# Performance work log

Measured on AMD Instinct MI355X. Metric: run time of the kernel, lower is better.

The kernel has to match this reference:

```python
import jax, jax.numpy as jnp
import numpy as np

N_HEAD = 16
N_EMBD = 1024
LOCAL_WINDOW = 256
GLOBAL_IDX = np.array([0, 1, 2, 3], dtype=np.int64)


def build_mask(T):
    # [T, T] boolean: local causal window + global rows/cols (Longformer-style)
    i = np.arange(T)[:, None]
    j = np.arange(T)[None, :]
    causal = j <= i
    local = causal & (j >= i - LOCAL_WINDOW + 1)
    g_row = np.isin(np.arange(T), GLOBAL_IDX)[:, None]  # global queries attend to all past
    g_col = np.isin(np.arange(T), GLOBAL_IDX)[None, :]  # global keys attended by all later
    mask = local | (g_row & causal) | (g_col & causal)
    return jnp.asarray(mask)


def setup_inputs() -> dict:
    key = jax.random.key(0)
    k1, k2, k3 = jax.random.split(key, 3)
    B, T, C = 2, 2048, N_EMBD
    x = jax.random.normal(k1, (B, T, C), dtype=jnp.float32)
    w_attn = jax.random.normal(k2, (3 * C, C), dtype=jnp.float32) * (1.0 / np.sqrt(C))
    w_proj = jax.random.normal(k3, (C, C), dtype=jnp.float32) * (1.0 / np.sqrt(C))
    return {"x": x, "w_attn": w_attn, "w_proj": w_proj}


def reference(x, w_attn, w_proj):
    B, T, C = x.shape
    H, D = N_HEAD, C // N_HEAD
    qkv = jnp.einsum('btc,fc->btf', x, w_attn)  # [B,T,3C], torch Linear: x @ W.T
    q, k, v = jnp.split(qkv, 3, axis=-1)
    # [B,H,T,D]
    q = q.reshape(B, T, H, D).transpose(0, 2, 1, 3)
    k = k.reshape(B, T, H, D).transpose(0, 2, 1, 3)
    v = v.reshape(B, T, H, D).transpose(0, 2, 1, 3)
    mask = build_mask(T)  # [T,T] bool, constant
    scale = 1.0 / np.sqrt(D)
    att = jnp.einsum('bhqd,bhkd->bhqk', q, k) * scale
    att = jnp.where(mask, att, jnp.finfo(att.dtype).min)
    att = jax.nn.softmax(att, axis=-1)
    y = jnp.einsum('bhqk,bhkd->bhqd', att, v)
    y = y.transpose(0, 2, 1, 3).reshape(B, T, C)
    return jnp.einsum('btc,oc->bto', y, w_proj)
```

## Files before the change

kernel.cpp:

```cpp
#include <hip/hip_runtime.h>


#define NHD   16
#define CEMB  1024
#define C3    3072
#define DH    64
#define WIN   256
#define NGLB  4
#define TB    256

typedef __attribute__((ext_vector_type(8))) short  short8v;
typedef __attribute__((ext_vector_type(4))) float  f32x4;
typedef __attribute__((ext_vector_type(8))) unsigned short ushort8v;

__device__ __forceinline__ unsigned short f2bf_rn(float f) {
    unsigned int u = __float_as_uint(f);
    u += 0x7fffu + ((u >> 16) & 1u);
    return (unsigned short)(u >> 16);
}
__device__ __forceinline__ float bf2f(unsigned short h) {
    return __uint_as_float(((unsigned int)h) << 16);
}

__global__ __launch_bounds__(TB)
void split3_kernel(const float* __restrict__ x, const float* __restrict__ wa,
                   const float* __restrict__ wp,
                   unsigned short* __restrict__ xh, unsigned short* __restrict__ xl,
                   unsigned short* __restrict__ wah, unsigned short* __restrict__ wal,
                   unsigned short* __restrict__ wph, unsigned short* __restrict__ wpl,
                   int n8x, int n8a, int n8p) {
    const int total = n8x + n8a + n8p;
    for (int i = blockIdx.x * blockDim.x + threadIdx.x; i < total;
         i += gridDim.x * blockDim.x) {
        const float* src; unsigned short *ph, *pl; int j;
        if (i < n8x)            { src = x;  ph = xh;  pl = xl;  j = i; }
        else if (i < n8x + n8a) { src = wa; ph = wah; pl = wal; j = i - n8x; }
        else                    { src = wp; ph = wph; pl = wpl; j = i - n8x - n8a; }
        float4 v0 = ((const float4*)src)[2 * j];
        float4 v1 = ((const float4*)src)[2 * j + 1];
        float f[8] = {v0.x, v0.y, v0.z, v0.w, v1.x, v1.y, v1.z, v1.w};
        ushort8v h, l;
#pragma unroll
        for (int e = 0; e < 8; ++e) {
            unsigned short hb = f2bf_rn(f[e]);
            h[e] = hb;
            l[e] = f2bf_rn(f[e] - bf2f(hb));
        }
        *(ushort8v*)&ph[(size_t)j * 8] = h;
        *(ushort8v*)&pl[(size_t)j * 8] = l;
    }
}

__device__ __forceinline__ void g2l16(const void* g, void* l) {
    __builtin_amdgcn_global_load_lds(
        (const __attribute__((address_space(1))) void*)g,
        (__attribute__((address_space(3))) void*)l, 16, 0, 0);
}

template<int OUTMODE>
__global__ __launch_bounds__(TB)
void gemm_split_mfma_kernel(const unsigned short* __restrict__ Ah,
                            const unsigned short* __restrict__ Al,
                            const unsigned short* __restrict__ Bh,
                            const unsigned short* __restrict__ Bl,
                            float* __restrict__ Cf,
                            unsigned short* __restrict__ Ch,
                            unsigned short* __restrict__ Cl,
                            int M, int N, int K) {
    __shared__ unsigned short lds[2][4][128 * 32];

    const int tid  = threadIdx.x;
    const int wave = tid >> 6;
    const int lane = tid & 63;
    const int nbn  = N >> 7;
    const int mb   = blockIdx.x / nbn;
    const int nb   = blockIdx.x % nbn;

    const int row0 = (wave)     * 16 + (lane >> 2);
    const int row1 = (wave + 4) * 16 + (lane >> 2);
    const int koff = (((lane & 3) ^ ((lane >> 3) & 3)) << 3);
    const size_t aoff0 = (size_t)(mb * 128 + row0) * K + koff;
    const size_t aoff1 = (size_t)(mb * 128 + row1) * K + koff;
    const size_t boff0 = (size_t)(nb * 128 + row0) * K + koff;
    const size_t boff1 = (size_t)(nb * 128 + row1) * K + koff;
    const int l0 = wave * 512;
    const int l1 = (wave + 4) * 512;

    const int wr = wave >> 1, wc = wave & 1;
    const int fr = lane & 15;
    const int g  = lane >> 4;
    const int ksel = (fr >> 1) & 3;

    f32x4 acc[4][4];
#pragma unroll
    for (int m = 0; m < 4; ++m)
#pragma unroll
        for (int n = 0; n < 4; ++n) acc[m][n] = (f32x4){0.f, 0.f, 0.f, 0.f};

    auto STAGE = [&](int bi, int kt) {
        g2l16(Ah + aoff0 + kt, &lds[bi][0][l0]);
        g2l16(Ah + aoff1 + kt, &lds[bi][0][l1]);
        g2l16(Al + aoff0 + kt, &lds[bi][1][l0]);
        g2l16(Al + aoff1 + kt, &lds[bi][1][l1]);
        g2l16(Bh + boff0 + kt, &lds[bi][2][l0]);
        g2l16(Bh + boff1 + kt, &lds[bi][2][l1]);
        g2l16(Bl + boff0 + kt, &lds[bi][3][l0]);
        g2l16(Bl + boff1 + kt, &lds[bi][3][l1]);
    };

    STAGE(0, 0);
    __syncthreads();
    int cur = 0;

    for (int kt = 0; kt < K; kt += 32) {
        if (kt + 32 < K) STAGE(cur ^ 1, kt + 32);

        const int co = ((g ^ ksel) << 3);
        short8v ah[4], al[4], bh[4], bl[4];
#pragma unroll
        for (int m = 0; m < 4; ++m) {
            const int r = (wr * 64 + m * 16 + fr) * 32 + co;
            ah[m] = *(const short8v*)&lds[cur][0][r];
            al[m] = *(const short8v*)&lds[cur][1][r];
        }
#pragma unroll
        for (int n = 0; n < 4; ++n) {
            const int r = (wc * 64 + n * 16 + fr) * 32 + co;
            bh[n] = *(const short8v*)&lds[cur][2][r];
            bl[n] = *(const short8v*)&lds[cur][3][r];
        }
#pragma unroll
        for (int m = 0; m < 4; ++m)
#pragma unroll
            for (int n = 0; n < 4; ++n) {
                acc[m][n] = __builtin_amdgcn_mfma_f32_16x16x32_bf16(
                    ah[m], bh[n], acc[m][n], 0, 0, 0);
                acc[m][n] = __builtin_amdgcn_mfma_f32_16x16x32_bf16(
                    ah[m], bl[n], acc[m][n], 0, 0, 0);
                acc[m][n] = __builtin_amdgcn_mfma_f32_16x16x32_bf16(
                    al[m], bh[n], acc[m][n], 0, 0, 0);
            }

        __syncthreads();
        cur ^= 1;
    }

    const int cr = (lane >> 4) * 4;
#pragma unroll
    for (int m = 0; m < 4; ++m)
#pragma unroll
        for (int n = 0; n < 4; ++n) {
#pragma unroll
            for (int r = 0; r < 4; ++r) {
                const int row = mb * 128 + wr * 64 + m * 16 + cr + r;
                const int col = nb * 128 + wc * 64 + n * 16 + fr;
                if constexpr (OUTMODE == 0) {
                    Cf[(size_t)row * N + col] = acc[m][n][r];
                } else {
                    float v = acc[m][n][r];
                    if (col < CEMB) v *= 0.125f;
                    unsigned short hb = f2bf_rn(v);
                    Ch[(size_t)row * N + col] = hb;
                    Cl[(size_t)row * N + col] = f2bf_rn(v - bf2f(hb));
                }
            }
        }
}

__global__ __launch_bounds__(TB)
void attn_mfma_kernel(const unsigned short* __restrict__ qkvh,
                      const unsigned short* __restrict__ qkvl,
                      unsigned short* __restrict__ yh,
                      unsigned short* __restrict__ yl, int T) {
    __shared__ unsigned short Kh[4096], Kl[4096], VTh[4096], VTl[4096],
                              Ph[4096], Pl[4096];

    const int tid = threadIdx.x;
    const int wv  = tid >> 6, ln = tid & 63;
    const int g   = ln >> 4, fr = ln & 15;
    const int nq  = T >> 6;
    const int qt  = blockIdx.x % nq;
    const int bh  = blockIdx.x / nq;
    const int h   = bh % NHD, b = bh / NHD;
    const int qs  = qt << 6;
    const size_t bT = (size_t)b * T;

    const size_t qbase = (bT + qs + wv * 16 + fr) * C3 + h * DH;
    short8v qfh[2], qfl[2];
    qfh[0] = *(const short8v*)(qkvh + qbase + g * 8);
    qfh[1] = *(const short8v*)(qkvh + qbase + 32 + g * 8);
    qfl[0] = *(const short8v*)(qkvl + qbase + g * 8);
    qfl[1] = *(const short8v*)(qkvl + qbase + 32 + g * 8);

    float mrow[4], lrow[4];
    f32x4 acc_o[4];
#pragma unroll
    for (int r = 0; r < 4; ++r) { mrow[r] = -3.0e38f; lrow[r] = 0.f; }
#pragma unroll
    for (int j = 0; j < 4; ++j) acc_o[j] = (f32x4){0.f, 0.f, 0.f, 0.f};

    int kt_first = 0;
    const int wstart = qs - (WIN - 1);
    if (wstart > 0) kt_first = wstart >> 6;
    const int has_g = (kt_first > 0) ? 1 : 0;
    const int npass = qt - kt_first + 1 + has_g;

    const int srow = tid >> 2;
    const int sc   = tid & 3;
    const int kidx0 = srow * 64 + ((sc * 8)       ^ ((srow & 7) << 3));
    const int kidx1 = srow * 64 + (((sc + 4) * 8) ^ ((srow & 7) << 3));

    short8v kh0, kh1, kl0, kl1, vh0, vh1, vl0, vl1;
    auto load_tile = [&](int k0) {
        const size_t kb = (bT + k0 + srow) * C3 + CEMB + h * DH;
        kh0 = *(const short8v*)(qkvh + kb + sc * 8);
        kh1 = *(const short8v*)(qkvh + kb + (sc + 4) * 8);
        kl0 = *(const short8v*)(qkvl + kb + sc * 8);
        kl1 = *(const short8v*)(qkvl + kb + (sc + 4) * 8);
        const size_t vb = (bT + k0 + srow) * C3 + 2 * CEMB + h * DH + sc * 16;
        vh0 = *(const short8v*)(qkvh + vb);
        vh1 = *(const short8v*)(qkvh + vb + 8);
        vl0 = *(const short8v*)(qkvl + vb);
        vl1 = *(const short8v*)(qkvl + vb + 8);
    };
    auto kt_of = [&](int p) { return (has_g && p == 0) ? 0 : (kt_first + p - has_g); };

    load_tile(kt_of(0) * 64);

    for (int pass = 0; pass < npass; ++pass) {
        const int k0 = kt_of(pass) * 64;

        __syncthreads();
        *(short8v*)&Kh[kidx0] = kh0; *(short8v*)&Kh[kidx1] = kh1;
        *(short8v*)&Kl[kidx0] = kl0; *(short8v*)&Kl[kidx1] = kl1;
#pragma unroll
        for (int e = 0; e < 8; ++e) {
            const int d1 = sc * 16 + e, d2 = sc * 16 + 8 + e;
            const int i1 = d1 * 64 + (srow ^ (((d1 ^ (d1 >> 3)) & 7) << 3));
            const int i2 = d2 * 64 + (srow ^ (((d2 ^ (d2 >> 3)) & 7) << 3));
            VTh[i1] = (unsigned short)vh0[e]; VTh[i2] = (unsigned short)vh1[e];
            VTl[i1] = (unsigned short)vl0[e]; VTl[i2] = (unsigned short)vl1[e];
        }
        __syncthreads();

        if (pass + 1 < npass) load_tile(kt_of(pass + 1) * 64);

        f32x4 sa[4];
#pragma unroll
        for (int j = 0; j < 4; ++j) sa[j] = (f32x4){0.f, 0.f, 0.f, 0.f};
#pragma unroll
        for (int kk = 0; kk < 2; ++kk) {
#pragma unroll
            for (int j = 0; j < 4; ++j) {
                const int krow = j * 16 + fr;
                const int off  = (kk * 32 + g * 8) ^ ((krow & 7) << 3);
                short8v bhf = *(const short8v*)&Kh[krow * 64 + off];
                short8v blf = *(const short8v*)&Kl[krow * 64 + off];
                sa[j] = __builtin_amdgcn_mfma_f32_16x16x32_bf16(qfh[kk], bhf, sa[j], 0, 0, 0);
                sa[j] = __builtin_amdgcn_mfma_f32_16x16x32_bf16(qfh[kk], blf, sa[j], 0, 0, 0);
                sa[j] = __builtin_amdgcn_mfma_f32_16x16x32_bf16(qfl[kk], bhf, sa[j], 0, 0, 0);
            }
        }

#pragma unroll
        for (int r = 0; r < 4; ++r) {
            const int qloc = wv * 16 + g * 4 + r;
            const int qi   = qs + qloc;
            const int wlo  = qi - (WIN - 1);
            float mx = mrow[r];
            float s[4];
#pragma unroll
            for (int j = 0; j < 4; ++j) {
                const int kj = k0 + j * 16 + fr;
                const bool valid = (kj <= qi) && ((kj >= wlo) || (kj < NGLB));
                s[j] = valid ? sa[j][r] : -3.0e38f;
                mx = fmaxf(mx, s[j]);
            }
#pragma unroll
            for (int off = 1; off < 16; off <<= 1)
                mx = fmaxf(mx, __shfl_xor(mx, off, 64));
            const float alpha = __expf(mrow[r] - mx);
            float rsum = 0.f;
            unsigned short phv[4], plv[4];
#pragma unroll
            for (int j = 0; j < 4; ++j) {
                const float p = (s[j] > -1.0e38f) ? __expf(s[j] - mx) : 0.f;
                rsum += p;
                const unsigned short hb = f2bf_rn(p);
                phv[j] = hb; plv[j] = f2bf_rn(p - bf2f(hb));
            }
#pragma unroll
            for (int off = 1; off < 16; off <<= 1)
                rsum += __shfl_xor(rsum, off, 64);
            lrow[r] = lrow[r] * alpha + rsum;
            mrow[r] = mx;
#pragma unroll
            for (int j = 0; j < 4; ++j) {
                acc_o[j][r] *= alpha;
                const int key = j * 16 + fr;
                const int idx = qloc * 64 + (key ^ ((qloc & 7) << 3));
                Ph[idx] = phv[j]; Pl[idx] = plv[j];
            }
        }

#pragma unroll
        for (int kk = 0; kk < 2; ++kk) {
            const int qloc = wv * 16 + fr;
            const int poff = (kk * 32 + g * 8) ^ ((qloc & 7) << 3);
            short8v pah = *(const short8v*)&Ph[qloc * 64 + poff];
            short8v pal = *(const short8v*)&Pl[qloc * 64 + poff];
#pragma unroll
            for (int j = 0; j < 4; ++j) {
                const int d   = j * 16 + fr;
                const int voff = (kk * 32 + g * 8) ^ (((d ^ (d >> 3)) & 7) << 3);
                short8v vfh = *(const short8v*)&VTh[d * 64 + voff];
                short8v vfl = *(const short8v*)&VTl[d * 64 + voff];
                acc_o[j] = __builtin_amdgcn_mfma_f32_16x16x32_bf16(pah, vfh, acc_o[j], 0, 0, 0);
                acc_o[j] = __builtin_amdgcn_mfma_f32_16x16x32_bf16(pah, vfl, acc_o[j], 0, 0, 0);
                acc_o[j] = __builtin_amdgcn_mfma_f32_16x16x32_bf16(pal, vfh, acc_o[j], 0, 0, 0);
            }
        }
    }

    float inv[4];
#pragma unroll
    for (int r = 0; r < 4; ++r) inv[r] = 1.0f / lrow[r];
#pragma unroll
    for (int j = 0; j < 4; ++j)
#pragma unroll
        for (int r = 0; r < 4; ++r) {
            const float o = acc_o[j][r] * inv[r];
            const size_t yi = (bT + qs + wv * 16 + g * 4 + r) * (size_t)CEMB
                            + h * DH + j * 16 + fr;
            const unsigned short hb = f2bf_rn(o);
            yh[yi] = hb; yl[yi] = f2bf_rn(o - bf2f(hb));
        }
}

extern "C" void kernel_launch(void* const* d_in, const int* in_sizes, int n_in,
                              void* d_out, int out_size, void* d_ws, size_t ws_size,
                              hipStream_t stream) {
    const float* x      = (const float*)d_in[0];
    const float* w_attn = (const float*)d_in[1];
    const float* w_proj = (const float*)d_in[2];
    float* out = (float*)d_out;

    const int T = 2048;
    const int B = in_sizes[0] / (T * CEMB);
    const int M = B * T;

    unsigned short* qkvh = (unsigned short*)d_ws;
    unsigned short* qkvl = qkvh + (size_t)M * C3;
    unsigned short* yh   = qkvl + (size_t)M * C3;
    unsigned short* yl   = yh   + (size_t)M * CEMB;
    unsigned short* xh   = yl   + (size_t)M * CEMB;
    unsigned short* xl   = xh   + (size_t)M * CEMB;
    unsigned short* wah  = xl   + (size_t)M * CEMB;
    unsigned short* wal  = wah  + (size_t)C3 * CEMB;
    unsigned short* wph  = wal  + (size_t)C3 * CEMB;
    unsigned short* wpl  = wph  + (size_t)CEMB * CEMB;

    const int n8x = M * CEMB / 8;
    const int n8a = C3 * CEMB / 8;
    const int n8p = CEMB * CEMB / 8;
    split3_kernel<<<2048, TB, 0, stream>>>(x, w_attn, w_proj,
                                           xh, xl, wah, wal, wph, wpl,
                                           n8x, n8a, n8p);

    gemm_split_mfma_kernel<1><<<dim3((M / 128) * (C3 / 128)), dim3(TB), 0, stream>>>(
        xh, xl, wah, wal, nullptr, qkvh, qkvl, M, C3, CEMB);

    attn_mfma_kernel<<<dim3(B * NHD * (T / 64)), dim3(TB), 0, stream>>>(
        qkvh, qkvl, yh, yl, T);

    gemm_split_mfma_kernel<0><<<dim3((M / 128) * (CEMB / 128)), dim3(TB), 0, stream>>>(
        yh, yl, wph, wpl, out, nullptr, nullptr, M, CEMB, CEMB);
}
```

Baseline: 247.3 us.

## Narrow proj GEMM tile, add MFMA priority hints, defer row-sum reduction

```diff
diff --git a/kernel.cpp b/kernel.cpp
--- a/kernel.cpp
+++ b/kernel.cpp
@@ -57,7 +57,7 @@
         (__attribute__((address_space(3))) void*)l, 16, 0, 0);
 }
 
-template<int OUTMODE>
+template<int OUTMODE, int BN>
 __global__ __launch_bounds__(TB)
 void gemm_split_mfma_kernel(const unsigned short* __restrict__ Ah,
                             const unsigned short* __restrict__ Al,
@@ -67,12 +67,14 @@
                             unsigned short* __restrict__ Ch,
                             unsigned short* __restrict__ Cl,
                             int M, int N, int K) {
-    __shared__ unsigned short lds[2][4][128 * 32];
+    constexpr int NFR = BN / 32;
+    __shared__ unsigned short ldsA[2][2][128 * 32];
+    __shared__ unsigned short ldsB[2][2][BN * 32];
 
     const int tid  = threadIdx.x;
     const int wave = tid >> 6;
     const int lane = tid & 63;
-    const int nbn  = N >> 7;
+    const int nbn  = N / BN;
     const int mb   = blockIdx.x / nbn;
     const int nb   = blockIdx.x % nbn;
 
@@ -81,8 +83,8 @@
     const int koff = (((lane & 3) ^ ((lane >> 3) & 3)) << 3);
     const size_t aoff0 = (size_t)(mb * 128 + row0) * K + koff;
     const size_t aoff1 = (size_t)(mb * 128 + row1) * K + koff;
-    const size_t boff0 = (size_t)(nb * 128 + row0) * K + koff;
-    const size_t boff1 = (size_t)(nb * 128 + row1) * K + koff;
+    const size_t boff0 = (size_t)(nb * BN + row0) * K + koff;
+    const size_t boff1 = (size_t)(nb * BN + row1) * K + koff;
     const int l0 = wave * 512;
     const int l1 = (wave + 4) * 512;
 
@@ -91,21 +93,23 @@
     const int g  = lane >> 4;
     const int ksel = (fr >> 1) & 3;
 
-    f32x4 acc[4][4];
+    f32x4 acc[4][NFR];
 #pragma unroll
     for (int m = 0; m < 4; ++m)
 #pragma unroll
-        for (int n = 0; n < 4; ++n) acc[m][n] = (f32x4){0.f, 0.f, 0.f, 0.f};
+        for (int n = 0; n < NFR; ++n) acc[m][n] = (f32x4){0.f, 0.f, 0.f, 0.f};
 
     auto STAGE = [&](int bi, int kt) {
-        g2l16(Ah + aoff0 + kt, &lds[bi][0][l0]);
-        g2l16(Ah + aoff1 + kt, &lds[bi][0][l1]);
-        g2l16(Al + aoff0 + kt, &lds[bi][1][l0]);
-        g2l16(Al + aoff1 + kt, &lds[bi][1][l1]);
-        g2l16(Bh + boff0 + kt, &lds[bi][2][l0]);
-        g2l16(Bh + boff1 + kt, &lds[bi][2][l1]);
-        g2l16(Bl + boff0 + kt, &lds[bi][3][l0]);
-        g2l16(Bl + boff1 + kt, &lds[bi][3][l1]);
+        g2l16(Ah + aoff0 + kt, &ldsA[bi][0][l0]);
+        g2l16(Ah + aoff1 + kt, &ldsA[bi][0][l1]);
+        g2l16(Al + aoff0 + kt, &ldsA[bi][1][l0]);
+        g2l16(Al + aoff1 + kt, &ldsA[bi][1][l1]);
+        g2l16(Bh + boff0 + kt, &ldsB[bi][0][l0]);
+        g2l16(Bl + boff0 + kt, &ldsB[bi][1][l0]);
+        if constexpr (BN == 128) {
+            g2l16(Bh + boff1 + kt, &ldsB[bi][0][l1]);
+            g2l16(Bl + boff1 + kt, &ldsB[bi][1][l1]);
+        }
     };
 
     STAGE(0, 0);
@@ -116,23 +120,24 @@
         if (kt + 32 < K) STAGE(cur ^ 1, kt + 32);
 
         const int co = ((g ^ ksel) << 3);
-        short8v ah[4], al[4], bh[4], bl[4];
+        short8v ah[4], al[4], bh[NFR], bl[NFR];
 #pragma unroll
         for (int m = 0; m < 4; ++m) {
             const int r = (wr * 64 + m * 16 + fr) * 32 + co;
-            ah[m] = *(const short8v*)&lds[cur][0][r];
-            al[m] = *(const short8v*)&lds[cur][1][r];
-        }
-#pragma unroll
-        for (int n = 0; n < 4; ++n) {
-            const int r = (wc * 64 + n * 16 + fr) * 32 + co;
-            bh[n] = *(const short8v*)&lds[cur][2][r];
-            bl[n] = *(const short8v*)&lds[cur][3][r];
-        }
+            ah[m] = *(const short8v*)&ldsA[cur][0][r];
+            al[m] = *(const short8v*)&ldsA[cur][1][r];
+        }
+#pragma unroll
+        for (int n = 0; n < NFR; ++n) {
+            const int r = (wc * (BN / 2) + n * 16 + fr) * 32 + co;
+            bh[n] = *(const short8v*)&ldsB[cur][0][r];
+            bl[n] = *(const short8v*)&ldsB[cur][1][r];
+        }
+        __builtin_amdgcn_s_setprio(1);
 #pragma unroll
         for (int m = 0; m < 4; ++m)
 #pragma unroll
-            for (int n = 0; n < 4; ++n) {
+            for (int n = 0; n < NFR; ++n) {
                 acc[m][n] = __builtin_amdgcn_mfma_f32_16x16x32_bf16(
                     ah[m], bh[n], acc[m][n], 0, 0, 0);
                 acc[m][n] = __builtin_amdgcn_mfma_f32_16x16x32_bf16(
@@ -140,6 +145,7 @@
                 acc[m][n] = __builtin_amdgcn_mfma_f32_16x16x32_bf16(
                     al[m], bh[n], acc[m][n], 0, 0, 0);
             }
+        __builtin_amdgcn_s_setprio(0);
 
         __syncthreads();
         cur ^= 1;
@@ -149,11 +155,11 @@
 #pragma unroll
     for (int m = 0; m < 4; ++m)
 #pragma unroll
-        for (int n = 0; n < 4; ++n) {
+        for (int n = 0; n < NFR; ++n) {
 #pragma unroll
             for (int r = 0; r < 4; ++r) {
                 const int row = mb * 128 + wr * 64 + m * 16 + cr + r;
-                const int col = nb * 128 + wc * 64 + n * 16 + fr;
+                const int col = nb * BN + wc * (BN / 2) + n * 16 + fr;
                 if constexpr (OUTMODE == 0) {
                     Cf[(size_t)row * N + col] = acc[m][n][r];
                 } else {
@@ -248,6 +254,7 @@
         f32x4 sa[4];
 #pragma unroll
         for (int j = 0; j < 4; ++j) sa[j] = (f32x4){0.f, 0.f, 0.f, 0.f};
+        __builtin_amdgcn_s_setprio(1);
 #pragma unroll
         for (int kk = 0; kk < 2; ++kk) {
 #pragma unroll
@@ -261,6 +268,7 @@
                 sa[j] = __builtin_amdgcn_mfma_f32_16x16x32_bf16(qfl[kk], bhf, sa[j], 0, 0, 0);
             }
         }
+        __builtin_amdgcn_s_setprio(0);
 
 #pragma unroll
         for (int r = 0; r < 4; ++r) {
@@ -289,9 +297,6 @@
                 const unsigned short hb = f2bf_rn(p);
                 phv[j] = hb; plv[j] = f2bf_rn(p - bf2f(hb));
             }
-#pragma unroll
-            for (int off = 1; off < 16; off <<= 1)
-                rsum += __shfl_xor(rsum, off, 64);
             lrow[r] = lrow[r] * alpha + rsum;
             mrow[r] = mx;
 #pragma unroll
@@ -303,6 +308,7 @@
             }
         }
 
+        __builtin_amdgcn_s_setprio(1);
 #pragma unroll
         for (int kk = 0; kk < 2; ++kk) {
             const int qloc = wv * 16 + fr;
@@ -320,11 +326,18 @@
                 acc_o[j] = __builtin_amdgcn_mfma_f32_16x16x32_bf16(pal, vfh, acc_o[j], 0, 0, 0);
             }
         }
+        __builtin_amdgcn_s_setprio(0);
     }
 
     float inv[4];
 #pragma unroll
-    for (int r = 0; r < 4; ++r) inv[r] = 1.0f / lrow[r];
+    for (int r = 0; r < 4; ++r) {
+        float s = lrow[r];
+#pragma unroll
+        for (int off = 1; off < 16; off <<= 1)
+            s += __shfl_xor(s, off, 64);
+        inv[r] = 1.0f / s;
+    }
 #pragma unroll
     for (int j = 0; j < 4; ++j)
 #pragma unroll
@@ -367,12 +380,12 @@
                                            xh, xl, wah, wal, wph, wpl,
                                            n8x, n8a, n8p);
 
-    gemm_split_mfma_kernel<1><<<dim3((M / 128) * (C3 / 128)), dim3(TB), 0, stream>>>(
+    gemm_split_mfma_kernel<1, 128><<<dim3((M / 128) * (C3 / 128)), dim3(TB), 0, stream>>>(
         xh, xl, wah, wal, nullptr, qkvh, qkvl, M, C3, CEMB);
 
     attn_mfma_kernel<<<dim3(B * NHD * (T / 64)), dim3(TB), 0, stream>>>(
         qkvh, qkvl, yh, yl, T);
 
-    gemm_split_mfma_kernel<0><<<dim3((M / 128) * (CEMB / 128)), dim3(TB), 0, stream>>>(
+    gemm_split_mfma_kernel<0, 64><<<dim3((M / 128) * (CEMB / 64)), dim3(TB), 0, stream>>>(
         yh, yl, wph, wpl, out, nullptr, nullptr, M, CEMB, CEMB);
 }
```

Result: slower. 257.8 us (+4.2%).
